# Kernel tuning notes

Hardware: AMD Instinct MI355X
Metric: run time of the kernel (lower is better)

The kernel has to match this reference:

```python
import jax, jax.numpy as jnp
import numpy as np

FS = 30.0        # sampling rate
N = 512          # input_size (time samples)
BIN_RES = 0.001  # frequency resolution
C, S = 32, 256   # channel / spatial dims of x
F_LO, F_HI = 0.66, 2.5


def _chirp_consts():
    """Deterministic CZT constants, matching the torch module's construction."""
    freq_zoom = np.arange(F_LO, F_HI, BIN_RES, dtype=np.float64)
    M = len(freq_zoom)  # 1840
    dt = 1.0 / FS  # (t[-1]-t[0])/(N-1) == 1/fs for t = arange(N)/fs
    df = (freq_zoom[-1] - freq_zoom[0]) / (M - 1)
    # A (phase ramp) diagonal values: 2*pi*f0*(-k)*dt, k = 0..N-1
    k = np.arange(N)
    a_vals = 2.0 * np.pi * freq_zoom[0] * (-k) * dt
    a_cos = np.cos(a_vals).astype(np.float32)
    a_sin = np.sin(a_vals).astype(np.float32)
    # W chirp matrix: -2*pi*df*k*n*dt, k in [0,M), n in [0,N)
    kv = np.arange(M)[:, None]
    nv = np.arange(N)[None, :]
    w_vals = -2.0 * np.pi * df * kv * nv * dt
    W_real = np.cos(w_vals).astype(np.float32)
    W_imag = np.sin(w_vals).astype(np.float32)
    return W_real, W_imag, a_cos, a_sin


def setup_inputs() -> dict:
    key = jax.random.key(0)
    x = jax.random.normal(key, (N, C, S), dtype=jnp.float32)
    W_real, W_imag, a_cos, a_sin = _chirp_consts()
    return {
        "x": x,
        "W_real": jnp.asarray(W_real),
        "W_imag": jnp.asarray(W_imag),
        "a_cos": jnp.asarray(a_cos),
        "a_sin": jnp.asarray(a_sin),
    }


def reference(x, W_real, W_imag, a_cos, a_sin):
    # A is diagonal -> diag matmul == per-row broadcast scaling (same math).
    Ax_real = a_cos[:, None, None] * x  # [N, C, S]
    Ax_imag = a_sin[:, None, None] * x  # [N, C, S]
    Ax = jnp.concatenate([Ax_real, Ax_imag], axis=0)  # [2N, C, S]
    # Block chirp matrix [[Wr, -Wi], [Wi, Wr]] -> [2M, 2N]
    W = jnp.concatenate(
        [
            jnp.concatenate([W_real, -W_imag], axis=1),
            jnp.concatenate([W_imag, W_real], axis=1),
        ],
        axis=0,
    )
    W = jnp.clip(W, -1.0, 1.0)  # Hardtanh (no-op on cos/sin, kept for fidelity)
    X = jnp.einsum("ji,ics->jcs", W, Ax)  # [2M, C, S]
    return W, X
```

## Files before the change

kernel.cpp:

```cpp
#include <hip/hip_runtime.h>
#include <hip/hip_bf16.h>
#include <stdint.h>

#define MM   1840
#define M2   3680
#define NN   512
#define K2   1024
#define CS   8192
#define MPAD 3712

#define NB_M 29
#define NB_N 64

#define WPREP_BLOCKS (MPAD / 2)
#define XT_NB        (CS / 32)
#define XT_KB        (NN / 64)

typedef __bf16 bf16x8 __attribute__((ext_vector_type(8)));
typedef float  floatx4 __attribute__((ext_vector_type(4)));


__global__ __launch_bounds__(256) void czt_prep(const float* __restrict__ Wr,
                                                const float* __restrict__ Wi,
                                                const float* __restrict__ ac,
                                                const float* __restrict__ as_,
                                                const float* __restrict__ x,
                                                float* __restrict__ Wout,
                                                __hip_bfloat16* __restrict__ Abf,
                                                __hip_bfloat16* __restrict__ Bxt) {
    __shared__ float tile[64 * 33];
    const int b   = blockIdx.x;
    const int tid = threadIdx.x;

    if (b < WPREP_BLOCKS) {
        const int j = b * 2 + (tid >> 7);
        const int k = (tid & 127) * 4;

        union { __hip_bfloat16 h[4]; uint2 u; } p;
        if (j < M2) {
            const int jj = (j < MM) ? j : j - MM;
            const floatx4 wr = *(const floatx4*)&Wr[(size_t)jj * NN + k];
            const floatx4 wi = *(const floatx4*)&Wi[(size_t)jj * NN + k];
            const floatx4 c  = *(const floatx4*)&ac[k];
            const floatx4 s  = *(const floatx4*)&as_[k];
            floatx4 f, g;
            floatx4 a;
            if (j < MM) {
                f = wr;
                g = -wi;
                a = wr * c - wi * s;
            } else {
                f = wi;
                g = wr;
                a = wi * c + wr * s;
            }
#pragma unroll
            for (int e = 0; e < 4; ++e) {
                f[e] = fminf(1.f, fmaxf(-1.f, f[e]));
                g[e] = fminf(1.f, fmaxf(-1.f, g[e]));
            }
            *(floatx4*)&Wout[(size_t)j * K2 + k]      = f;
            *(floatx4*)&Wout[(size_t)j * K2 + NN + k] = g;
            p.h[0] = __float2bfloat16(a[0]);
            p.h[1] = __float2bfloat16(a[1]);
            p.h[2] = __float2bfloat16(a[2]);
            p.h[3] = __float2bfloat16(a[3]);
        } else {
            p.h[0] = p.h[1] = p.h[2] = p.h[3] = __float2bfloat16(0.0f);
        }
        *(uint2*)&Abf[(size_t)j * NN + k] = p.u;
    } else {
        const int tb = b - WPREP_BLOCKS;
        const int n0 = (tb & (XT_NB - 1)) * 32;
        const int k0 = (tb >> 8) * 64;

        const int row = tid >> 2;
        const int c8  = (tid & 3) * 8;
        const floatx4* src = (const floatx4*)&x[(size_t)(k0 + row) * CS + n0 + c8];
        const floatx4 v0 = src[0];
        const floatx4 v1 = src[1];
        float* tr = &tile[row * 33 + c8];
        tr[0] = v0[0]; tr[1] = v0[1]; tr[2] = v0[2]; tr[3] = v0[3];
        tr[4] = v1[0]; tr[5] = v1[1]; tr[6] = v1[2]; tr[7] = v1[3];
        __syncthreads();

        const int oc = tid & 7;
        const int nr = tid >> 3;
        union { __hip_bfloat16 h[8]; uint4 u; } q;
#pragma unroll
        for (int jj = 0; jj < 8; ++jj)
            q.h[jj] = __float2bfloat16(tile[(oc * 8 + jj) * 33 + nr]);
        *(uint4*)&Bxt[(size_t)(n0 + nr) * NN + k0 + oc * 8] = q.u;
    }
}

__device__ __forceinline__ void gload_lds16(const void* g, void* l) {
    __builtin_amdgcn_global_load_lds(
        (const __attribute__((address_space(1))) uint32_t*)g,
        (__attribute__((address_space(3))) uint32_t*)l,
        16, 0, 0);
}

__global__ __launch_bounds__(256) void czt_gemm(const __hip_bfloat16* __restrict__ Abf,
                                                const __hip_bfloat16* __restrict__ Bxt,
                                                float* __restrict__ Xout) {
    __shared__ __hip_bfloat16 As[128 * 64];
    __shared__ __hip_bfloat16 Bs[128 * 64];

    const int tid  = threadIdx.x;
    const int lane = tid & 63;
    const int w    = tid >> 6;
    const int quad = lane >> 4;
    const int r16  = lane & 15;

    const int b    = blockIdx.x;
    const int xcd  = b & 7;
    const int i    = b >> 3;
    const int mb   = i % NB_M;
    const int nl   = i / NB_M;
    const int mtile = mb * 128;
    const int ntile = (xcd * 8 + nl) * 128;

    const int wm = (w >> 1) * 64;
    const int wn = (w & 1) * 64;

    const int rsub   = lane >> 3;
    const int rstage = w * 32 + rsub;
    const int cstage = ((lane & 7) ^ rsub) * 8;
    const __hip_bfloat16* Ag = Abf + (size_t)(mtile + rstage) * NN + cstage;
    const __hip_bfloat16* Bg = Bxt + (size_t)(ntile + rstage) * NN + cstage;

    floatx4 acc[4][4] = {};

#pragma unroll
    for (int kt = 0; kt < NN / 64; ++kt) {
        __syncthreads();
#pragma unroll
        for (int t = 0; t < 4; ++t) {
            gload_lds16(Ag + (size_t)(t * 8) * NN + kt * 64, &As[(w * 32 + t * 8) * 64]);
            gload_lds16(Bg + (size_t)(t * 8) * NN + kt * 64, &Bs[(w * 32 + t * 8) * 64]);
        }
        __syncthreads();

#pragma unroll
        for (int ks = 0; ks < 2; ++ks) {
            bf16x8 af[4], bfr[4];
#pragma unroll
            for (int i2 = 0; i2 < 4; ++i2) {
                const int ra = wm + i2 * 16 + r16;
                const int rb = wn + i2 * 16 + r16;
                const int pa = ((ks * 4 + quad) ^ (r16 & 7)) * 8;
                af[i2]  = *(const bf16x8*)&As[ra * 64 + pa];
                bfr[i2] = *(const bf16x8*)&Bs[rb * 64 + pa];
            }
#pragma unroll
            for (int i2 = 0; i2 < 4; ++i2)
#pragma unroll
                for (int jn = 0; jn < 4; ++jn)
                    acc[i2][jn] = __builtin_amdgcn_mfma_f32_16x16x32_bf16(
                        af[i2], bfr[jn], acc[i2][jn], 0, 0, 0);
        }
    }

#pragma unroll
    for (int i2 = 0; i2 < 4; ++i2) {
        const int rbase = mtile + wm + i2 * 16 + quad * 4;
#pragma unroll
        for (int rr = 0; rr < 4; ++rr) {
            const int rg = rbase + rr;
            if (rg < M2) {
#pragma unroll
                for (int jn = 0; jn < 4; ++jn) {
                    const int cg = ntile + wn + jn * 16 + r16;
                    Xout[(size_t)rg * CS + cg] = acc[i2][jn][rr];
                }
            }
        }
    }
}

extern "C" void kernel_launch(void* const* d_in, const int* in_sizes, int n_in,
                              void* d_out, int out_size, void* d_ws, size_t ws_size,
                              hipStream_t stream) {
    const float* x   = (const float*)d_in[0];
    const float* Wr  = (const float*)d_in[1];
    const float* Wi  = (const float*)d_in[2];
    const float* ac  = (const float*)d_in[3];
    const float* as_ = (const float*)d_in[4];

    float* Wout = (float*)d_out;
    float* Xout = (float*)d_out + (size_t)M2 * K2;

    __hip_bfloat16* Abf = (__hip_bfloat16*)d_ws;
    __hip_bfloat16* Bxt = (__hip_bfloat16*)((char*)d_ws + (size_t)MPAD * NN * 2);

    czt_prep<<<dim3(WPREP_BLOCKS + XT_NB * XT_KB), dim3(256), 0, stream>>>(
        Wr, Wi, ac, as_, x, Wout, Abf, Bxt);
    czt_gemm<<<dim3(NB_M * NB_N), dim3(256), 0, stream>>>(Abf, Bxt, Xout);
}
```

Before: 183.8 us.

## Enlarge GEMM tiles to 256x256 with double-buffered LDS prefetch pipeline

Rewrites the bf16 MFMA GEMM to use 256x256 block tiles and 512 threads, with each wave computing 128x64. A and B tiles are double-buffered in LDS, and the stage two iterations ahead is prefetched through explicit vmcnt waits and raw barriers, with s_setprio around the MFMA bursts. The block-to-tile mapping is also remapped across XCDs. The aim is more data reuse per LDS load and overlap of global loads with compute. In exchange it uses more registers and LDS, launches far fewer blocks (480), and clamps A rows at the padding edge.

```diff
diff --git a/kernel.cpp b/kernel.cpp
--- a/kernel.cpp
+++ b/kernel.cpp
@@ -9,16 +9,18 @@
 #define CS   8192
 #define MPAD 3712
 
-#define NB_M 29
-#define NB_N 64
-
 #define WPREP_BLOCKS (MPAD / 2)
 #define XT_NB        (CS / 32)
 #define XT_KB        (NN / 64)
 
+#define GBM 256
+#define GBN 256
+#define NBM2 15
+#define NBN2 32
+#define NKT  8
+
 typedef __bf16 bf16x8 __attribute__((ext_vector_type(8)));
 typedef float  floatx4 __attribute__((ext_vector_type(4)));
-
 
 __global__ __launch_bounds__(256) void czt_prep(const float* __restrict__ Wr,
                                                 const float* __restrict__ Wi,
@@ -43,17 +45,9 @@
             const floatx4 wi = *(const floatx4*)&Wi[(size_t)jj * NN + k];
             const floatx4 c  = *(const floatx4*)&ac[k];
             const floatx4 s  = *(const floatx4*)&as_[k];
-            floatx4 f, g;
-            floatx4 a;
-            if (j < MM) {
-                f = wr;
-                g = -wi;
-                a = wr * c - wi * s;
-            } else {
-                f = wi;
-                g = wr;
-                a = wi * c + wr * s;
-            }
+            floatx4 f, g, a;
+            if (j < MM) { f = wr; g = -wi; a = wr * c - wi * s; }
+            else        { f = wi; g = wr;  a = wi * c + wr * s; }
 #pragma unroll
             for (int e = 0; e < 4; ++e) {
                 f[e] = fminf(1.f, fmaxf(-1.f, f[e]));
@@ -101,11 +95,22 @@
         16, 0, 0);
 }
 
-__global__ __launch_bounds__(256) void czt_gemm(const __hip_bfloat16* __restrict__ Abf,
-                                                const __hip_bfloat16* __restrict__ Bxt,
-                                                float* __restrict__ Xout) {
-    __shared__ __hip_bfloat16 As[128 * 64];
-    __shared__ __hip_bfloat16 Bs[128 * 64];
+__device__ __forceinline__ void raw_bar() {
+    __builtin_amdgcn_sched_barrier(0);
+    asm volatile("s_barrier" ::: "memory");
+    __builtin_amdgcn_sched_barrier(0);
+}
+
+__device__ __forceinline__ void wait_lgkm0() {
+    asm volatile("s_waitcnt lgkmcnt(0)" ::: "memory");
+    __builtin_amdgcn_sched_barrier(0);
+}
+
+__global__ __launch_bounds__(512, 2) void czt_gemm(const __hip_bfloat16* __restrict__ Abf,
+                                                   const __hip_bfloat16* __restrict__ Bxt,
+                                                   float* __restrict__ Xout) {
+    __shared__ __hip_bfloat16 As[2][GBM * 64];
+    __shared__ __hip_bfloat16 Bs[2][GBN * 64];
 
     const int tid  = threadIdx.x;
     const int lane = tid & 63;
@@ -113,66 +118,102 @@
     const int quad = lane >> 4;
     const int r16  = lane & 15;
 
-    const int b    = blockIdx.x;
-    const int xcd  = b & 7;
-    const int i    = b >> 3;
-    const int mb   = i % NB_M;
-    const int nl   = i / NB_M;
-    const int mtile = mb * 128;
-    const int ntile = (xcd * 8 + nl) * 128;
-
-    const int wm = (w >> 1) * 64;
-    const int wn = (w & 1) * 64;
+    const int b  = blockIdx.x;
+    const int wk = (b & 7) * 60 + (b >> 3);
+    const int mb = wk % NBM2;
+    const int nb = wk / NBM2;
+    const int mtile = mb * GBM;
+    const int ntile = nb * GBN;
+
+    const int wm = (w >> 2) * 128;
+    const int wn = (w & 3) * 64;
 
     const int rsub   = lane >> 3;
-    const int rstage = w * 32 + rsub;
     const int cstage = ((lane & 7) ^ rsub) * 8;
-    const __hip_bfloat16* Ag = Abf + (size_t)(mtile + rstage) * NN + cstage;
-    const __hip_bfloat16* Bg = Bxt + (size_t)(ntile + rstage) * NN + cstage;
-
-    floatx4 acc[4][4] = {};
-
-#pragma unroll
-    for (int kt = 0; kt < NN / 64; ++kt) {
-        __syncthreads();
-#pragma unroll
-        for (int t = 0; t < 4; ++t) {
-            gload_lds16(Ag + (size_t)(t * 8) * NN + kt * 64, &As[(w * 32 + t * 8) * 64]);
-            gload_lds16(Bg + (size_t)(t * 8) * NN + kt * 64, &Bs[(w * 32 + t * 8) * 64]);
-        }
-        __syncthreads();
-
-#pragma unroll
-        for (int ks = 0; ks < 2; ++ks) {
-            bf16x8 af[4], bfr[4];
-#pragma unroll
-            for (int i2 = 0; i2 < 4; ++i2) {
-                const int ra = wm + i2 * 16 + r16;
-                const int rb = wn + i2 * 16 + r16;
-                const int pa = ((ks * 4 + quad) ^ (r16 & 7)) * 8;
-                af[i2]  = *(const bf16x8*)&As[ra * 64 + pa];
-                bfr[i2] = *(const bf16x8*)&Bs[rb * 64 + pa];
-            }
-#pragma unroll
-            for (int i2 = 0; i2 < 4; ++i2)
-#pragma unroll
-                for (int jn = 0; jn < 4; ++jn)
-                    acc[i2][jn] = __builtin_amdgcn_mfma_f32_16x16x32_bf16(
-                        af[i2], bfr[jn], acc[i2][jn], 0, 0, 0);
+
+#define STAGE(kt_, bf_)                                                          \
+    do {                                                                         \
+        _Pragma("unroll")                                                        \
+        for (int t4 = 0; t4 < 4; ++t4) {                                         \
+            const int rs = w * 32 + t4 * 8;                    \
+            int ar = mtile + rs + rsub;                                          \
+            if (ar > MPAD - 1) ar = MPAD - 1;           \
+            gload_lds16(Abf + (size_t)ar * NN + (kt_) * 64 + cstage,             \
+                        &As[(bf_)][rs * 64]);                                    \
+            gload_lds16(Bxt + (size_t)(ntile + rs + rsub) * NN + (kt_) * 64 +    \
+                            cstage,                                              \
+                        &Bs[(bf_)][rs * 64]);                                    \
+        }                                                                        \
+    } while (0)
+
+    floatx4 acc[8][4] = {};
+
+    STAGE(0, 0);
+    STAGE(1, 1);
+
+#pragma unroll
+    for (int t = 0; t < NKT; ++t) {
+        if (t < NKT - 1) asm volatile("s_waitcnt vmcnt(8)" ::: "memory");
+        else             asm volatile("s_waitcnt vmcnt(0)" ::: "memory");
+        __builtin_amdgcn_sched_barrier(0);
+        raw_bar();
+        const int bf_ = t & 1;
+
+        {
+            const int pch = ((0 * 4 + quad) ^ (r16 & 7)) * 8;
+            bf16x8 af[8], bv[4];
+#pragma unroll
+            for (int m = 0; m < 8; ++m)
+                af[m] = *(const bf16x8*)&As[bf_][(wm + m * 16 + r16) * 64 + pch];
+#pragma unroll
+            for (int n = 0; n < 4; ++n)
+                bv[n] = *(const bf16x8*)&Bs[bf_][(wn + n * 16 + r16) * 64 + pch];
+            wait_lgkm0();
+            __builtin_amdgcn_s_setprio(1);
+#pragma unroll
+            for (int m = 0; m < 8; ++m)
+#pragma unroll
+                for (int n = 0; n < 4; ++n)
+                    acc[m][n] = __builtin_amdgcn_mfma_f32_16x16x32_bf16(
+                        af[m], bv[n], acc[m][n], 0, 0, 0);
+            __builtin_amdgcn_s_setprio(0);
+        }
+
+        {
+            const int pch = ((1 * 4 + quad) ^ (r16 & 7)) * 8;
+            bf16x8 af[8], bv[4];
+#pragma unroll
+            for (int m = 0; m < 8; ++m)
+                af[m] = *(const bf16x8*)&As[bf_][(wm + m * 16 + r16) * 64 + pch];
+#pragma unroll
+            for (int n = 0; n < 4; ++n)
+                bv[n] = *(const bf16x8*)&Bs[bf_][(wn + n * 16 + r16) * 64 + pch];
+            wait_lgkm0();
+            raw_bar();
+            if (t + 2 < NKT) STAGE(t + 2, bf_);
+            __builtin_amdgcn_s_setprio(1);
+#pragma unroll
+            for (int m = 0; m < 8; ++m)
+#pragma unroll
+                for (int n = 0; n < 4; ++n)
+                    acc[m][n] = __builtin_amdgcn_mfma_f32_16x16x32_bf16(
+                        af[m], bv[n], acc[m][n], 0, 0, 0);
+            __builtin_amdgcn_s_setprio(0);
         }
     }
-
-#pragma unroll
-    for (int i2 = 0; i2 < 4; ++i2) {
-        const int rbase = mtile + wm + i2 * 16 + quad * 4;
+#undef STAGE
+
+#pragma unroll
+    for (int m = 0; m < 8; ++m) {
+        const int rbase = mtile + wm + m * 16 + quad * 4;
 #pragma unroll
         for (int rr = 0; rr < 4; ++rr) {
             const int rg = rbase + rr;
             if (rg < M2) {
 #pragma unroll
-                for (int jn = 0; jn < 4; ++jn) {
-                    const int cg = ntile + wn + jn * 16 + r16;
-                    Xout[(size_t)rg * CS + cg] = acc[i2][jn][rr];
+                for (int n = 0; n < 4; ++n) {
+                    const int cg = ntile + wn + n * 16 + r16;
+                    Xout[(size_t)rg * CS + cg] = acc[m][n][rr];
                 }
             }
         }
@@ -196,5 +237,5 @@
 
     czt_prep<<<dim3(WPREP_BLOCKS + XT_NB * XT_KB), dim3(256), 0, stream>>>(
         Wr, Wi, ac, as_, x, Wout, Abf, Bxt);
-    czt_gemm<<<dim3(NB_M * NB_N), dim3(256), 0, stream>>>(Abf, Bxt, Xout);
-}
+    czt_gemm<<<dim3(NBM2 * NBN2), dim3(512), 0, stream>>>(Abf, Bxt, Xout);
+}
```

Result: no change. 184.6 us (+0.4%).
